# Kernel tuning notes

Hardware: AMD Instinct MI355X
Metric: run time of the kernel (lower is better)

## Reference

```python
import jax, jax.numpy as jnp
import numpy as np

D_MODEL = 512
N_HEADS = 8
HEAD_DIM = D_MODEL // N_HEADS
SEQ = 2048
BATCH = 2
EPS = 1e-5
SCALE = 1.0 / np.sqrt(HEAD_DIM).astype(np.float32)
# (kind, window, dilation) per head, matching init_kwargs head_specs
SPECS = [("global", 0, 1), ("global", 0, 1),
         ("window", 64, 1), ("window", 128, 1), ("window", 256, 1),
         ("dilated", 64, 2), ("dilated", 64, 4), ("dilated", 64, 8)]


def build_masks(N):
    i = jnp.arange(N)
    D = jnp.abs(i[:, None] - i[None, :])
    ms = []
    for kind, w, dil in SPECS:
        if kind == "global":
            ms.append(jnp.ones((N, N), dtype=bool))
        elif kind == "window":
            ms.append(D <= w)
        else:  # dilated
            ms.append((D % dil == 0) & (D // dil <= w))
    return jnp.stack(ms)  # [H, N, N] bool


def layernorm(x, g, b):
    mu = jnp.mean(x, axis=-1, keepdims=True)
    var = jnp.mean((x - mu) ** 2, axis=-1, keepdims=True)
    return (x - mu) * jax.lax.rsqrt(var + EPS) * g + b


def setup_inputs() -> dict:
    key = jax.random.key(0)
    ks = jax.random.split(key, 7)
    w = 0.02
    return {
        "x": jax.random.normal(ks[0], (BATCH, SEQ, D_MODEL), dtype=jnp.float32),
        "Wq": jax.random.normal(ks[1], (D_MODEL, D_MODEL), dtype=jnp.float32) * w,
        "Wk": jax.random.normal(ks[2], (D_MODEL, D_MODEL), dtype=jnp.float32) * w,
        "Wv": jax.random.normal(ks[3], (D_MODEL, D_MODEL), dtype=jnp.float32) * w,
        "Wo": jax.random.normal(ks[4], (D_MODEL, D_MODEL), dtype=jnp.float32) * w,
        "T_w1": jax.random.normal(ks[5], (D_MODEL, D_MODEL), dtype=jnp.float32) * w,
        "T_b1": jnp.zeros((D_MODEL,), dtype=jnp.float32),
        "T_w2": jax.random.normal(ks[6], (1, D_MODEL), dtype=jnp.float32) * w,
        "T_b2": jnp.zeros((1,), dtype=jnp.float32),
        "ln_in_g": jnp.ones((D_MODEL,), dtype=jnp.float32),
        "ln_in_b": jnp.zeros((D_MODEL,), dtype=jnp.float32),
        "ln_out_g": jnp.ones((D_MODEL,), dtype=jnp.float32),
        "ln_out_b": jnp.zeros((D_MODEL,), dtype=jnp.float32),
    }


def reference(x, Wq, Wk, Wv, Wo, T_w1, T_b1, T_w2, T_b2,
              ln_in_g, ln_in_b, ln_out_g, ln_out_b):
    B, N, H = x.shape
    x0 = x
    xn = layernorm(x, ln_in_g, ln_in_b)
    # torch Linear: y = x @ W.T ; reshape to [B, h, N, d]
    def heads(W):
        return (xn @ W.T).reshape(B, N, N_HEADS, HEAD_DIM).transpose(0, 2, 1, 3)
    Q, K, V = heads(Wq), heads(Wk), heads(Wv)
    attn = jnp.einsum("bhqd,bhkd->bhqk", Q, K) * SCALE
    mask = build_masks(N)  # [h, N, N]
    attn = jnp.where(mask[None], attn, -jnp.inf)
    attn = jax.nn.softmax(attn, axis=-1)  # every row has diagonal unmasked
    out = jnp.einsum("bhqk,bhkd->bhqd", attn, V)
    out = out.transpose(0, 2, 1, 3).reshape(B, N, N_HEADS * HEAD_DIM)
    out = out @ Wo.T
    # tanh-gated softmax over sequence dim
    T_logits = jnp.tanh(xn @ T_w1.T + T_b1) @ T_w2.T + T_b2  # [B, N, 1]
    T = jax.nn.softmax(T_logits, axis=1)
    out = out * T
    return layernorm(out + x0, ln_out_g, ln_out_b)
```

## Files before the change

### kernel.cpp

```cpp
#include <hip/hip_runtime.h>
#include <math.h>

#define N_SEQ 2048
#define DM    512
#define NTOK  4096
#define NH    8
#define HD    64
#define NSLOT 18

typedef __attribute__((ext_vector_type(8))) short short8;
typedef __attribute__((ext_vector_type(4))) short short4_t;
typedef __attribute__((ext_vector_type(4))) float f32x4;

__device__ inline short f2bf(float x) {
    union { float f; unsigned u; } v; v.f = x;
    unsigned r = v.u + 0x7fff + ((v.u >> 16) & 1);
    return (short)(r >> 16);
}
__device__ inline float bf2f(short s) {
    union { unsigned u; float f; } v; v.u = ((unsigned)(unsigned short)s) << 16;
    return v.f;
}
__device__ inline unsigned pkbf(float a, float b) {
    return ((unsigned)(unsigned short)f2bf(b) << 16) | (unsigned)(unsigned short)f2bf(a);
// ... 32 lines not shown
        __shared__ float ls[4], lq[4];
        if ((t & 63) == 0) { ls[t >> 6] = s; lq[t >> 6] = q; }
        __syncthreads();
        s = ls[sub * 2] + ls[sub * 2 + 1];
        q = lq[sub * 2] + lq[sub * 2 + 1];
        float mu = s * (1.f / DM);
        float var = q * (1.f / DM) - mu * mu;
        float rs = rsqrtf(var + 1e-5f);
        float4 gv = ((const float4*)g)[tt], bv = ((const float4*)b)[tt];
        short4_t o;
        o[0] = f2bf((xv.x - mu) * rs * gv.x + bv.x);
        o[1] = f2bf((xv.y - mu) * rs * gv.y + bv.y);
        o[2] = f2bf((xv.z - mu) * rs * gv.z + bv.z);
        o[3] = f2bf((xv.w - mu) * rs * gv.w + bv.w);
        *(short4_t*)&y[(size_t)tk * DM + tt * 4] = o;
    } else {
        int id = (blk - 2048) * 256 + t;
        if (id < 262144) {
            int z = id >> 16; int off = id & 65535;
            const float* s = (z == 0) ? Wq : (z == 1) ? Wk : (z == 2) ? Wv : Tw1;
            float4 v = ((const float4*)s)[off];
            short4_t o = {f2bf(v.x), f2bf(v.y), f2bf(v.z), f2bf(v.w)};
            *(short4_t*)(wcat + (size_t)z * 262144 + (size_t)off * 4) = o;
        } else {
            int off = id - 262144;
            float4 v = ((const float4*)Wo)[off];
            short4_t o = {f2bf(v.x), f2bf(v.y), f2bf(v.z), f2bf(v.w)};
            *(short4_t*)(wo + (size_t)off * 4) = o;
        }
    }
}

__global__ __launch_bounds__(256) void k_gemmqkvt(
    const short* __restrict__ A, const short* __restrict__ W,
    const float* __restrict__ Tb1, const float* __restrict__ Tw2,
    short* __restrict__ qb, short* __restrict__ kb, short* __restrict__ vtb,
    float* __restrict__ lg) {
    __shared__ short smem[17408];
    int t = threadIdx.x;
    int lane = t & 63, w = t >> 6;
    int wy = w >> 1, wx = w & 1;
    int ln = lane & 15, q4 = lane >> 4;
    int c0 = blockIdx.x * 128, m0 = blockIdx.y * 128;
    int sr = t >> 2, sc = (t & 3) << 3;
    f32x4 acc[4][4];
    f32x4 zero = {0.f, 0.f, 0.f, 0.f};
    #pragma unroll
    for (int i = 0; i < 4; i++)
        #pragma unroll
        for (int j = 0; j < 4; j++) acc[i][j] = zero;
    {
        short* AsB = smem; short* BsB = smem + 4096;
        async_cp16(&A[(size_t)(m0 + sr) * DM + sc],      &AsB[sr * 32 + sc]);
        async_cp16(&A[(size_t)(m0 + 64 + sr) * DM + sc], &AsB[(64 + sr) * 32 + sc]);
        async_cp16(&W[(size_t)(c0 + sr) * DM + sc],      &BsB[sr * 32 + sc]);
        async_cp16(&W[(size_t)(c0 + 64 + sr) * DM + sc], &BsB[(64 + sr) * 32 + sc]);
    }
    __syncthreads();
    for (int kk = 0; kk < 16; kk++) {
        short* AsB = &smem[(kk & 1) * 8192];
        short* BsB = AsB + 4096;
        if (kk < 15) {
            short* AsN = &smem[((kk & 1) ^ 1) * 8192];
            short* BsN = AsN + 4096;
            int k0 = (kk + 1) * 32;
            async_cp16(&A[(size_t)(m0 + sr) * DM + k0 + sc],      &AsN[sr * 32 + sc]);
            async_cp16(&A[(size_t)(m0 + 64 + sr) * DM + k0 + sc], &AsN[(64 + sr) * 32 + sc]);
            async_cp16(&W[(size_t)(c0 + sr) * DM + k0 + sc],      &BsN[sr * 32 + sc]);
            async_cp16(&W[(size_t)(c0 + 64 + sr) * DM + k0 + sc], &BsN[(64 + sr) * 32 + sc]);
        }
        short8 af[4], bfr[4];
        #pragma unroll
        for (int i = 0; i < 4; i++)
            af[i] = *(short8*)&AsB[(wy * 64 + i * 16 + ln) * 32 + q4 * 8];
        #pragma unroll
        for (int j = 0; j < 4; j++)
            bfr[j] = *(short8*)&BsB[(wx * 64 + j * 16 + ln) * 32 + q4 * 8];
        #pragma unroll
        for (int i = 0; i < 4; i++)
            #pragma unroll
            for (int j = 0; j < 4; j++)
                acc[i][j] = mfma16(af[i], bfr[j], acc[i][j]);
        __syncthreads();
    }
    short* Es = smem;
    int z = c0 >> 9;
    int bi = m0 >> 11, n0 = m0 & (N_SEQ - 1);
    int hp = (c0 & 511) >> 6;
    if (z < 2) {
        short* dst0 = (z == 0) ? qb : kb;
        float sc2 = (z == 0) ? 0.125f : 1.0f;
        #pragma unroll
        for (int i = 0; i < 4; i++)
            #pragma unroll
            for (int j = 0; j < 4; j++)
                #pragma unroll
                for (int r = 0; r < 4; r++) {
                    int nl = wy * 64 + i * 16 + q4 * 4 + r;
                    int cl = wx * 64 + j * 16 + ln;
                    Es[nl * 136 + cl] = f2bf(acc[i][j][r] * sc2);
                }
        __syncthreads();
        #pragma unroll
        for (int ii = 0; ii < 8; ii++) {
            int id = t + 256 * ii;
            int nl = id >> 4, c8 = id & 15;
            short8 v = *(short8*)&Es[nl * 136 + c8 * 8];
            int hh = hp + (c8 >> 3), d8 = (c8 & 7) * 8;
            *(short8*)&dst0[(((size_t)bi * NH + hh) * N_SEQ + n0 + nl) * HD + d8] = v;
        }
    } else if (z == 2) {
        #pragma unroll
        for (int i = 0; i < 4; i++)
            #pragma unroll
            for (int j = 0; j < 4; j++) {
                int nl0 = wy * 64 + i * 16 + q4 * 4;
                int dl = wx * 64 + j * 16 + ln;
                *(unsigned*)&Es[dl * 136 + nl0]     = pkbf(acc[i][j][0], acc[i][j][1]);
                *(unsigned*)&Es[dl * 136 + nl0 + 2] = pkbf(acc[i][j][2], acc[i][j][3]);
            }
        __syncthreads();
        #pragma unroll
        for (int ii = 0; ii < 8; ii++) {
            int id = t + 256 * ii;
            int dl = id >> 4, nc = id & 15;
            short8 v = *(short8*)&Es[dl * 136 + nc * 8];
            int h = hp + (dl >> 6), d = dl & 63;
            *(short8*)&vtb[(((size_t)bi * NH + h) * HD + d) * N_SEQ + n0 + nc * 8] = v;
        }
    } else {
        #pragma unroll
        for (int i = 0; i < 4; i++) {
            #pragma unroll
            for (int r = 0; r < 4; r++) {
                float s = 0.f;
                #pragma unroll
                for (int j = 0; j < 4; j++) {
                    int tc = (c0 & 511) + wx * 64 + j * 16 + ln;
                    s += ftanh(acc[i][j][r] + Tb1[tc]) * Tw2[tc];
                }
                s += __shfl_xor(s, 1);
                s += __shfl_xor(s, 2);
                s += __shfl_xor(s, 4);
                s += __shfl_xor(s, 8);
                if (ln == 0) {
                    int row = m0 + wy * 64 + i * 16 + q4 * 4 + r;
                    atomicAdd(&lg[row], s);
                }
            }
        }
    }
}

__global__ __launch_bounds__(256) void k_gemmp(
    const short* __restrict__ A, const short* __restrict__ W,
    float* __restrict__ proj) {
    __shared__ short smem[12288];
    int t = threadIdx.x;
    int lane = t & 63, w = t >> 6;
    int wy = w >> 1, wx = w & 1;
    int ln = lane & 15, q4 = lane >> 4;
    int c0 = blockIdx.x * 64, m0 = blockIdx.y * 128;
    int sr = t >> 2, sc = (t & 3) << 3;
    f32x4 acc[4][2];
    f32x4 zero = {0.f, 0.f, 0.f, 0.f};
    #pragma unroll
    for (int i = 0; i < 4; i++) { acc[i][0] = zero; acc[i][1] = zero; }
    {
        short* AsB = smem; short* BsB = smem + 4096;
        async_cp16(&A[(size_t)(m0 + sr) * DM + sc],      &AsB[sr * 32 + sc]);
        async_cp16(&A[(size_t)(m0 + 64 + sr) * DM + sc], &AsB[(64 + sr) * 32 + sc]);
        async_cp16(&W[(size_t)(c0 + sr) * DM + sc],      &BsB[sr * 32 + sc]);
    }
    __syncthreads();
    for (int kk = 0; kk < 16; kk++) {
        short* AsB = &smem[(kk & 1) * 6144];
        short* BsB = AsB + 4096;
        if (kk < 15) {
            short* AsN = &smem[((kk & 1) ^ 1) * 6144];
            short* BsN = AsN + 4096;
            int k0 = (kk + 1) * 32;
            async_cp16(&A[(size_t)(m0 + sr) * DM + k0 + sc],      &AsN[sr * 32 + sc]);
            async_cp16(&A[(size_t)(m0 + 64 + sr) * DM + k0 + sc], &AsN[(64 + sr) * 32 + sc]);
            async_cp16(&W[(size_t)(c0 + sr) * DM + k0 + sc],      &BsN[sr * 32 + sc]);
        }
        short8 af[4], bfr[2];
        #pragma unroll
        for (int i = 0; i < 4; i++)
            af[i] = *(short8*)&AsB[(wy * 64 + i * 16 + ln) * 32 + q4 * 8];
        #pragma unroll
        for (int j = 0; j < 2; j++)
            bfr[j] = *(short8*)&BsB[(wx * 32 + j * 16 + ln) * 32 + q4 * 8];
        #pragma unroll
        for (int i = 0; i < 4; i++)
            #pragma unroll
            for (int j = 0; j < 2; j++)
                acc[i][j] = mfma16(af[i], bfr[j], acc[i][j]);
        __syncthreads();
    }
    #pragma unroll
    for (int i = 0; i < 4; i++)
        #pragma unroll
        for (int j = 0; j < 2; j++)
            #pragma unroll
            for (int r = 0; r < 4; r++) {
                int row = m0 + wy * 64 + i * 16 + q4 * 4 + r;
                int col = c0 + wx * 32 + j * 16 + ln;
                proj[(size_t)row * DM + col] = acc[i][j][r];
            }
}

__global__ __launch_bounds__(256) void k_attn(const short* __restrict__ qb,
                                              const short* __restrict__ kb,
                                              const short* __restrict__ vtb,
                                              short* __restrict__ P_O,
                                              float* __restrict__ P_ml,
                                              short* __restrict__ ob,
                                              const float* __restrict__ lg,
                                              float* __restrict__ gate) {
    __shared__ short Ks[128 * 64];
    __shared__ short Vt[64 * 128];
    __shared__ short Pa[4][16 * 136];
    __shared__ float rg[8];
    int t = threadIdx.x;
    int lane = t & 63, w = t >> 6;
    int ln = lane & 15, q4 = lane >> 4;
    int slot = blockIdx.x, qt = blockIdx.y, bi = blockIdx.z;
    int q0 = qt * 64;
    int h, c;
    if (slot < 4)        { h = 0; c = slot; }
    else if (slot < 8)   { h = 1; c = slot - 4; }
    else if (slot == 8)  { h = 2; c = 0; }
    else if (slot == 9)  { h = 3; c = 0; }
    else if (slot < 12)  { h = 4; c = slot - 10; }
    else if (slot == 12) { h = 5; c = 0; }
    else if (slot < 15)  { h = 6; c = slot - 13; }
    else                 { h = 7; c = slot - 15; }
    int solo = (slot == 8) | (slot == 9) | (slot == 12);
    int kind = (h < 2) ? 0 : (h < 5) ? 1 : 2;
    int wnd = (h == 2 || h >= 5) ? 64 : (h == 3) ? 128 : (h == 4) ? 256 : 0;
    int dsh = (h == 5) ? 1 : (h == 6) ? 2 : (h == 7) ? 3 : 0;
    int dmask = (1 << dsh) - 1;
    int wmax = (kind == 0) ? 0 : (wnd << dsh);
    int tLoU, tHiU, CS;
    if (kind == 0) { tLoU = 0; tHiU = 15; CS = 4; }
    else { tLoU = (q0 - wmax) >> 7; tHiU = (q0 + 63 + wmax) >> 7; CS = 3; }
    int ktLo = tLoU + c * CS;
    int ktHi = ktLo + CS - 1;
    if (ktHi > tHiU) ktHi = tHiU;
    if (ktHi > 15) ktHi = 15;
    if (ktLo < 0) ktLo = 0;
    int p4 = (bi * 32 + qt) * NSLOT + slot;
    float* ml = P_ml + (size_t)p4 * 128;
    if (ktLo > ktHi) {
        if (t < 64) { ml[t] = -1e30f; ml[64 + t] = 0.f; }
        return;
    }
    const size_t base = ((size_t)bi * NH + h) * N_SEQ * HD;
    const short* Q = qb + base;
    const short* K = kb + base;
    const short* Vg = vtb + base;
    short8 qa[2];
    {
        const short* qrow = Q + (size_t)(q0 + w * 16 + ln) * HD + q4 * 8;
        qa[0] = *(const short8*)qrow;
        qa[1] = *(const short8*)(qrow + 32);
    }
    int qi = q0 + w * 16 + ln;
    float m_i = -1e30f, l_i = 0.f;
    f32x4 OT[4];
    f32x4 zero = {0.f, 0.f, 0.f, 0.f};
    #pragma unroll
    for (int d = 0; d < 4; d++) OT[d] = zero;
    short* Paw = Pa[w];
    for (int kt = ktLo; kt <= ktHi; kt++) {
        int k0 = kt << 7;
        __syncthreads();
        #pragma unroll
        for (int i2 = 0; i2 < 4; i2++) {
            int id = t + 256 * i2;
            int kr = id >> 3, ck = id & 7;
            async_cp16(&K[(size_t)(k0 + kr) * HD + ((ck ^ (kr & 7)) << 3)],
                       &Ks[id << 3]);
            int dr = id >> 4, cv = id & 15;
            async_cp16(&Vg[(size_t)dr * N_SEQ + k0 + ((cv ^ (dr & 15)) << 3)],
                       &Vt[id << 3]);
        }
        __syncthreads();
        f32x4 ST[8];
        #pragma unroll
        for (int nt = 0; nt < 8; nt++) ST[nt] = zero;
        __builtin_amdgcn_s_setprio(1);
        #pragma unroll
        for (int nt = 0; nt < 8; nt++) {
            #pragma unroll
            for (int ks = 0; ks < 2; ks++) {
                int cc = ((ks * 4 + q4) ^ (ln & 7)) << 3;
                short8 af = *(short8*)&Ks[(nt * 16 + ln) * 64 + cc];
                ST[nt] = mfma16(af, qa[ks], ST[nt]);
            }
        }
        __builtin_amdgcn_s_setprio(0);
        if (kind != 0) {
            #pragma unroll
            for (int nt = 0; nt < 8; nt++)
                #pragma unroll
                for (int r = 0; r < 4; r++) {
                    int key = k0 + nt * 16 + q4 * 4 + r;
                    int dlt = qi - key; dlt = (dlt < 0) ? -dlt : dlt;
                    int valid;
                    if (kind == 1) valid = (dlt <= wnd);
                    else valid = ((dlt & dmask) == 0) && ((dlt >> dsh) <= wnd);
                    if (!valid) ST[nt][r] = -1e30f;
                }
        }
        float rm = -1e30f;
        #pragma unroll
        for (int nt = 0; nt < 8; nt++) {
            float a = fmaxf(ST[nt][0], ST[nt][1]);
            float b = fmaxf(ST[nt][2], ST[nt][3]);
            rm = fmaxf(rm, fmaxf(a, b));
        }
        rm = fmaxf(rm, __shfl_xor(rm, 16));
        rm = fmaxf(rm, __shfl_xor(rm, 32));
        float mn = fmaxf(m_i, rm);
        float sc = __expf(m_i - mn);
        float rs = 0.f;
        #pragma unroll
        for (int nt = 0; nt < 8; nt++) {
            float p0 = __expf(ST[nt][0] - mn);
            float p1 = __expf(ST[nt][1] - mn);
            float p2 = __expf(ST[nt][2] - mn);
            float p3 = __expf(ST[nt][3] - mn);
            rs += (p0 + p1) + (p2 + p3);
            *(unsigned*)&Paw[ln * 136 + nt * 16 + q4 * 4]     = pkbf(p0, p1);
            *(unsigned*)&Paw[ln * 136 + nt * 16 + q4 * 4 + 2] = pkbf(p2, p3);
        }
        rs += __shfl_xor(rs, 16);
        rs += __shfl_xor(rs, 32);
        l_i = l_i * sc + rs;
        m_i = mn;
        #pragma unroll
        for (int d = 0; d < 4; d++) OT[d] *= sc;
        short8 pb[4];
        #pragma unroll
        for (int ks = 0; ks < 4; ks++)
            pb[ks] = *(short8*)&Paw[ln * 136 + ks * 32 + q4 * 8];
        __builtin_amdgcn_s_setprio(1);
        #pragma unroll
        for (int dt = 0; dt < 4; dt++) {
            #pragma unroll
            for (int ks = 0; ks < 4; ks++) {
                int cc = ((ks * 4 + q4) ^ ln) << 3;
                short8 a = *(short8*)&Vt[(dt * 16 + ln) * 128 + cc];
                OT[dt] = mfma16(a, pb[ks], OT[dt]);
            }
        }
        __builtin_amdgcn_s_setprio(0);
    }
    if (solo) {
        float inv = 1.f / l_i;
        #pragma unroll
        for (int dt = 0; dt < 4; dt++) {
            *(unsigned*)&Paw[ln * 136 + dt * 16 + q4 * 4]     = pkbf(OT[dt][0] * inv, OT[dt][1] * inv);
            *(unsigned*)&Paw[ln * 136 + dt * 16 + q4 * 4 + 2] = pkbf(OT[dt][2] * inv, OT[dt][3] * inv);
        }
        short8 o0 = *(short8*)&Paw[ln * 136 + q4 * 16];
        short8 o1 = *(short8*)&Paw[ln * 136 + q4 * 16 + 8];
        short* dst = ob + ((size_t)bi * N_SEQ + q0 + w * 16 + ln) * DM + h * 64 + q4 * 16;
        *(short8*)dst = o0;
        *(short8*)(dst + 8) = o1;
    } else {
        if (q4 == 0) { ml[w * 16 + ln] = m_i; ml[64 + w * 16 + ln] = l_i; }
        #pragma unroll
        for (int dt = 0; dt < 4; dt++) {
            *(unsigned*)&Paw[ln * 136 + dt * 16 + q4 * 4]     = pkbf(OT[dt][0], OT[dt][1]);
            *(unsigned*)&Paw[ln * 136 + dt * 16 + q4 * 4 + 2] = pkbf(OT[dt][2], OT[dt][3]);
        }
        short8 o0 = *(short8*)&Paw[ln * 136 + q4 * 16];
        short8 o1 = *(short8*)&Paw[ln * 136 + q4 * 16 + 8];
        short* Op = P_O + (size_t)p4 * 4096;
        *(short8*)&Op[(w * 16 + ln) * 64 + q4 * 16] = o0;
        *(short8*)&Op[(w * 16 + ln) * 64 + q4 * 16 + 8] = o1;
    }
    if (slot == 8 && qt == 0) {
        int b = bi;
        float v[8];
        float4 a0 = *(const float4*)&lg[b * N_SEQ + t * 8];
        float4 a1 = *(const float4*)&lg[b * N_SEQ + t * 8 + 4];
        v[0] = a0.x; v[1] = a0.y; v[2] = a0.z; v[3] = a0.w;
        v[4] = a1.x; v[5] = a1.y; v[6] = a1.z; v[7] = a1.w;
        float m = v[0];
        #pragma unroll
        for (int j = 1; j < 8; j++) m = fmaxf(m, v[j]);
        for (int o = 32; o; o >>= 1) m = fmaxf(m, __shfl_down(m, o));
        if ((t & 63) == 0) rg[t >> 6] = m;
        __syncthreads();
        m = fmaxf(fmaxf(rg[0], rg[1]), fmaxf(rg[2], rg[3]));
        float e[8], s = 0.f;
        #pragma unroll
        for (int j = 0; j < 8; j++) { e[j] = __expf(v[j] - m); s += e[j]; }
        for (int o = 32; o; o >>= 1) s += __shfl_down(s, o);
        if ((t & 63) == 0) rg[4 + (t >> 6)] = s;
        __syncthreads();
        s = (rg[4] + rg[5]) + (rg[6] + rg[7]);
        float inv = 1.f / s;
        float4 o0 = {e[0] * inv, e[1] * inv, e[2] * inv, e[3] * inv};
        float4 o1 = {e[4] * inv, e[5] * inv, e[6] * inv, e[7] * inv};
        *(float4*)&gate[b * N_SEQ + t * 8] = o0;
        *(float4*)&gate[b * N_SEQ + t * 8 + 4] = o1;
    }
}

__global__ __launch_bounds__(256) void k_combine(const short* __restrict__ P_O,
                                                 const float* __restrict__ P_ml,
                                                 short* __restrict__ ob) {
    const int hsel[5]  = {0, 1, 4, 6, 7};
    const int hbase[5] = {0, 4, 10, 13, 15};
    const int hcnt[5]  = {4, 4, 2, 2, 3};
    int hh = blockIdx.x, qt = blockIdx.y, bi = blockIdx.z;
    int h = hsel[hh];
    int t = threadIdx.x;
    int row = t >> 2, c0 = (t & 3) * 16;
    int pb = (bi * 32 + qt) * NSLOT + hbase[hh];
    int cnt = hcnt[hh];
    float m = -1e30f;
    for (int s = 0; s < cnt; s++)
        m = fmaxf(m, P_ml[(size_t)(pb + s) * 128 + row]);
    float l = 0.f;
    float acc[16];
    #pragma unroll
    for (int j = 0; j < 16; j++) acc[j] = 0.f;
    for (int s = 0; s < cnt; s++) {
        float ms = P_ml[(size_t)(pb + s) * 128 + row];
        float ls = P_ml[(size_t)(pb + s) * 128 + 64 + row];
        if (ls > 0.f) {
            float sc = __expf(ms - m);
            l += ls * sc;
            const short* Op = P_O + (size_t)(pb + s) * 4096 + row * 64 + c0;
            short8 v0 = *(const short8*)Op;
            short8 v1 = *(const short8*)(Op + 8);
            #pragma unroll
            for (int j = 0; j < 8; j++) acc[j]     += bf2f(v0[j]) * sc;
            #pragma unroll
            for (int j = 0; j < 8; j++) acc[8 + j] += bf2f(v1[j]) * sc;
        }
    }
    float inv = 1.f / l;
    int n = qt * 64 + row;
    short8 o0, o1;
    #pragma unroll
    for (int j = 0; j < 8; j++) o0[j] = f2bf(acc[j] * inv);
    #pragma unroll
    for (int j = 0; j < 8; j++) o1[j] = f2bf(acc[8 + j] * inv);
    short* dst = ob + ((size_t)bi * N_SEQ + n) * DM + h * 64 + c0;
    *(short8*)dst = o0;
    *(short8*)(dst + 8) = o1;
}

__global__ __launch_bounds__(128) void k_final(const float* __restrict__ proj,
                                               const float* __restrict__ gate,
                                               const float* __restrict__ x0,
                                               const float* __restrict__ g,
                                               const float* __restrict__ b,
                                               float* __restrict__ out) {
    int tk = blockIdx.x, t = threadIdx.x;
    float gt = gate[tk];
    float4 pv = ((const float4*)(proj + (size_t)tk * DM))[t];
    float4 xv = ((const float4*)(x0 + (size_t)tk * DM))[t];
    float4 y;
    y.x = pv.x * gt + xv.x;
    y.y = pv.y * gt + xv.y;
    y.z = pv.z * gt + xv.z;
    y.w = pv.w * gt + xv.w;
    float s = y.x + y.y + y.z + y.w;
    float q = y.x*y.x + y.y*y.y + y.z*y.z + y.w*y.w;
    for (int o = 32; o; o >>= 1) { s += __shfl_down(s, o); q += __shfl_down(q, o); }
    __shared__ float ls[2], lq[2];
    if ((t & 63) == 0) { ls[t >> 6] = s; lq[t >> 6] = q; }
    __syncthreads();
    s = ls[0] + ls[1]; q = lq[0] + lq[1];
    float mu = s * (1.f / DM);
    float var = q * (1.f / DM) - mu * mu;
    float rs = rsqrtf(var + 1e-5f);
    float4 gv = ((const float4*)g)[t], bv = ((const float4*)b)[t];
    float4 o;
    o.x = (y.x - mu) * rs * gv.x + bv.x;
    o.y = (y.y - mu) * rs * gv.y + bv.y;
    o.z = (y.z - mu) * rs * gv.z + bv.z;
    o.w = (y.w - mu) * rs * gv.w + bv.w;
    ((float4*)(out + (size_t)tk * DM))[t] = o;
}

extern "C" void kernel_launch(void* const* d_in, const int* in_sizes, int n_in,
                              void* d_out, int out_size, void* d_ws, size_t ws_size,
                              hipStream_t stream) {
    (void)in_sizes; (void)n_in; (void)out_size; (void)ws_size;
    const float* x    = (const float*)d_in[0];
    const float* Wq   = (const float*)d_in[1];
    const float* Wk   = (const float*)d_in[2];
    const float* Wv   = (const float*)d_in[3];
    const float* Wo   = (const float*)d_in[4];
    const float* Tw1  = (const float*)d_in[5];
    const float* Tb1  = (const float*)d_in[6];
    const float* Tw2  = (const float*)d_in[7];
    const float* ling = (const float*)d_in[9];
    const float* linb = (const float*)d_in[10];
    const float* logg = (const float*)d_in[11];
    const float* logb = (const float*)d_in[12];
    float* out = (float*)d_out;

    const size_t SZ = (size_t)NTOK * DM;
    const int NPART = 2 * 32 * NSLOT;
    char* p = (char*)d_ws;
    short* xn   = (short*)p; p += SZ * 2;
    short* wcat = (short*)p; p += (size_t)2048 * DM * 2;
    short* wo   = (short*)p; p += (size_t)DM * DM * 2;
    short* qb   = (short*)p; p += SZ * 2;
    short* kb   = (short*)p; p += SZ * 2;
    short* vtb  = (short*)p; p += SZ * 2;
    short* obuf = (short*)p; p += SZ * 2;
    float* lg   = (float*)p; p += (size_t)NTOK * 4;
    float* gate = (float*)p; p += (size_t)NTOK * 4;
    float* P_ml = (float*)p; p += (size_t)NPART * 128 * 4;
    float* proj = (float*)p;
    short* P_O  = (short*)p; p += (size_t)NPART * 4096 * 2;

    k_lncvt<<<3328, 256, 0, stream>>>(x, ling, linb, xn, lg,
                                      Wq, Wk, Wv, Tw1, Wo, wcat, wo);
    k_gemmqkvt<<<dim3(16, 32), 256, 0, stream>>>(xn, wcat, Tb1, Tw2,
                                                 qb, kb, vtb, lg);
    k_attn<<<dim3(NSLOT, 32, 2), 256, 0, stream>>>(qb, kb, vtb, P_O, P_ml,
                                                   obuf, lg, gate);
    k_combine<<<dim3(5, 32, 2), 256, 0, stream>>>(P_O, P_ml, obuf);
    k_gemmp<<<dim3(8, 32), 256, 0, stream>>>(obuf, wo, proj);
    k_final<<<NTOK, 128, 0, stream>>>(proj, gate, x, logg, logb, out);
}
```

Before: 154.5 us.

## Fuse split-KV combine, output projection, gating and final layernorm into one kernel

Drops the separate combine, output-projection GEMM and final layernorm kernels and replaces them with a single kernel. Each 512-thread block merges the partial attention results for 64 rows across all heads into shared memory, multiplies them by Wo, applies the gate and residual, and performs the layernorm in registers. Solo-head attention slots no longer write normalized output directly; they now write partials like the other slots. This removes two launches and the obuf/proj round trips through global memory. The cost is that the fused kernel runs only 64 blocks with a large shared-memory footprint, so GPU occupancy and parallelism drop sharply.

```diff
diff --git a/kernel.cpp b/kernel.cpp
--- a/kernel.cpp
+++ b/kernel.cpp
@@ -208,70 +208,11 @@
     }
 }
 
-__global__ __launch_bounds__(256) void k_gemmp(
-    const short* __restrict__ A, const short* __restrict__ W,
-    float* __restrict__ proj) {
-    __shared__ short smem[12288];
-    int t = threadIdx.x;
-    int lane = t & 63, w = t >> 6;
-    int wy = w >> 1, wx = w & 1;
-    int ln = lane & 15, q4 = lane >> 4;
-    int c0 = blockIdx.x * 64, m0 = blockIdx.y * 128;
-    int sr = t >> 2, sc = (t & 3) << 3;
-    f32x4 acc[4][2];
-    f32x4 zero = {0.f, 0.f, 0.f, 0.f};
-    #pragma unroll
-    for (int i = 0; i < 4; i++) { acc[i][0] = zero; acc[i][1] = zero; }
-    {
-        short* AsB = smem; short* BsB = smem + 4096;
-        async_cp16(&A[(size_t)(m0 + sr) * DM + sc],      &AsB[sr * 32 + sc]);
-        async_cp16(&A[(size_t)(m0 + 64 + sr) * DM + sc], &AsB[(64 + sr) * 32 + sc]);
-        async_cp16(&W[(size_t)(c0 + sr) * DM + sc],      &BsB[sr * 32 + sc]);
-    }
-    __syncthreads();
-    for (int kk = 0; kk < 16; kk++) {
-        short* AsB = &smem[(kk & 1) * 6144];
-        short* BsB = AsB + 4096;
-        if (kk < 15) {
-            short* AsN = &smem[((kk & 1) ^ 1) * 6144];
-            short* BsN = AsN + 4096;
-            int k0 = (kk + 1) * 32;
-            async_cp16(&A[(size_t)(m0 + sr) * DM + k0 + sc],      &AsN[sr * 32 + sc]);
-            async_cp16(&A[(size_t)(m0 + 64 + sr) * DM + k0 + sc], &AsN[(64 + sr) * 32 + sc]);
-            async_cp16(&W[(size_t)(c0 + sr) * DM + k0 + sc],      &BsN[sr * 32 + sc]);
-        }
-        short8 af[4], bfr[2];
-        #pragma unroll
-        for (int i = 0; i < 4; i++)
-            af[i] = *(short8*)&AsB[(wy * 64 + i * 16 + ln) * 32 + q4 * 8];
-        #pragma unroll
-        for (int j = 0; j < 2; j++)
-            bfr[j] = *(short8*)&BsB[(wx * 32 + j * 16 + ln) * 32 + q4 * 8];
-        #pragma unroll
-        for (int i = 0; i < 4; i++)
-            #pragma unroll
-            for (int j = 0; j < 2; j++)
-                acc[i][j] = mfma16(af[i], bfr[j], acc[i][j]);
-        __syncthreads();
-    }
-    #pragma unroll
-    for (int i = 0; i < 4; i++)
-        #pragma unroll
-        for (int j = 0; j < 2; j++)
-            #pragma unroll
-            for (int r = 0; r < 4; r++) {
-                int row = m0 + wy * 64 + i * 16 + q4 * 4 + r;
-                int col = c0 + wx * 32 + j * 16 + ln;
-                proj[(size_t)row * DM + col] = acc[i][j][r];
-            }
-}
-
 __global__ __launch_bounds__(256) void k_attn(const short* __restrict__ qb,
                                               const short* __restrict__ kb,
                                               const short* __restrict__ vtb,
                                               short* __restrict__ P_O,
                                               float* __restrict__ P_ml,
-                                              short* __restrict__ ob,
                                               const float* __restrict__ lg,
                                               float* __restrict__ gate) {
     __shared__ short Ks[128 * 64];
@@ -292,7 +233,6 @@
     else if (slot == 12) { h = 5; c = 0; }
     else if (slot < 15)  { h = 6; c = slot - 13; }
     else                 { h = 7; c = slot - 15; }
-    int solo = (slot == 8) | (slot == 9) | (slot == 12);
     int kind = (h < 2) ? 0 : (h < 5) ? 1 : 2;
     int wnd = (h == 2 || h >= 5) ? 64 : (h == 3) ? 128 : (h == 4) ? 256 : 0;
     int dsh = (h == 5) ? 1 : (h == 6) ? 2 : (h == 7) ? 3 : 0;
@@ -308,125 +248,114 @@
     if (ktLo < 0) ktLo = 0;
     int p4 = (bi * 32 + qt) * NSLOT + slot;
     float* ml = P_ml + (size_t)p4 * 128;
-    if (ktLo > ktHi) {
+    int empty = (ktLo > ktHi);
+    if (empty) {
         if (t < 64) { ml[t] = -1e30f; ml[64 + t] = 0.f; }
-        return;
+        if (!(slot == 8 && qt == 0)) return;
     }
     const size_t base = ((size_t)bi * NH + h) * N_SEQ * HD;
     const short* Q = qb + base;
     const short* K = kb + base;
     const short* Vg = vtb + base;
-    short8 qa[2];
-    {
-        const short* qrow = Q + (size_t)(q0 + w * 16 + ln) * HD + q4 * 8;
-        qa[0] = *(const short8*)qrow;
-        qa[1] = *(const short8*)(qrow + 32);
-    }
-    int qi = q0 + w * 16 + ln;
-    float m_i = -1e30f, l_i = 0.f;
-    f32x4 OT[4];
-    f32x4 zero = {0.f, 0.f, 0.f, 0.f};
-    #pragma unroll
-    for (int d = 0; d < 4; d++) OT[d] = zero;
-    short* Paw = Pa[w];
-    for (int kt = ktLo; kt <= ktHi; kt++) {
-        int k0 = kt << 7;
-        __syncthreads();
-        #pragma unroll
-        for (int i2 = 0; i2 < 4; i2++) {
-            int id = t + 256 * i2;
-            int kr = id >> 3, ck = id & 7;
-            async_cp16(&K[(size_t)(k0 + kr) * HD + ((ck ^ (kr & 7)) << 3)],
-                       &Ks[id << 3]);
-            int dr = id >> 4, cv = id & 15;
-            async_cp16(&Vg[(size_t)dr * N_SEQ + k0 + ((cv ^ (dr & 15)) << 3)],
-                       &Vt[id << 3]);
-        }
-        __syncthreads();
-        f32x4 ST[8];
-        #pragma unroll
-        for (int nt = 0; nt < 8; nt++) ST[nt] = zero;
-        __builtin_amdgcn_s_setprio(1);
-        #pragma unroll
-        for (int nt = 0; nt < 8; nt++) {
-            #pragma unroll
-            for (int ks = 0; ks < 2; ks++) {
-                int cc = ((ks * 4 + q4) ^ (ln & 7)) << 3;
-                short8 af = *(short8*)&Ks[(nt * 16 + ln) * 64 + cc];
-                ST[nt] = mfma16(af, qa[ks], ST[nt]);
-            }
-        }
-        __builtin_amdgcn_s_setprio(0);
-        if (kind != 0) {
-            #pragma unroll
-            for (int nt = 0; nt < 8; nt++)
+    if (!empty) {
+        short8 qa[2];
+        {
+            const short* qrow = Q + (size_t)(q0 + w * 16 + ln) * HD + q4 * 8;
+            qa[0] = *(const short8*)qrow;
+            qa[1] = *(const short8*)(qrow + 32);
+        }
+        int qi = q0 + w * 16 + ln;
+        float m_i = -1e30f, l_i = 0.f;
+        f32x4 OT[4];
+        f32x4 zero = {0.f, 0.f, 0.f, 0.f};
+        #pragma unroll
+        for (int d = 0; d < 4; d++) OT[d] = zero;
+        short* Paw = Pa[w];
+        for (int kt = ktLo; kt <= ktHi; kt++) {
+            int k0 = kt << 7;
+            __syncthreads();
+            #pragma unroll
+            for (int i2 = 0; i2 < 4; i2++) {
+                int id = t + 256 * i2;
+                int kr = id >> 3, ck = id & 7;
+                async_cp16(&K[(size_t)(k0 + kr) * HD + ((ck ^ (kr & 7)) << 3)],
+                           &Ks[id << 3]);
+                int dr = id >> 4, cv = id & 15;
+                async_cp16(&Vg[(size_t)dr * N_SEQ + k0 + ((cv ^ (dr & 15)) << 3)],
+                           &Vt[id << 3]);
+            }
+            __syncthreads();
+            f32x4 ST[8];
+            #pragma unroll
+            for (int nt = 0; nt < 8; nt++) ST[nt] = zero;
+            __builtin_amdgcn_s_setprio(1);
+            #pragma unroll
+            for (int nt = 0; nt < 8; nt++) {
                 #pragma unroll
-                for (int r = 0; r < 4; r++) {
-                    int key = k0 + nt * 16 + q4 * 4 + r;
-                    int dlt = qi - key; dlt = (dlt < 0) ? -dlt : dlt;
-                    int valid;
-                    if (kind == 1) valid = (dlt <= wnd);
-                    else valid = ((dlt & dmask) == 0) && ((dlt >> dsh) <= wnd);
-                    if (!valid) ST[nt][r] = -1e30f;
+                for (int ks = 0; ks < 2; ks++) {
+                    int cc = ((ks * 4 + q4) ^ (ln & 7)) << 3;
+                    short8 af = *(short8*)&Ks[(nt * 16 + ln) * 64 + cc];
+                    ST[nt] = mfma16(af, qa[ks], ST[nt]);
                 }
-        }
-        float rm = -1e30f;
-        #pragma unroll
-        for (int nt = 0; nt < 8; nt++) {
-            float a = fmaxf(ST[nt][0], ST[nt][1]);
-            float b = fmaxf(ST[nt][2], ST[nt][3]);
-            rm = fmaxf(rm, fmaxf(a, b));
-        }
-        rm = fmaxf(rm, __shfl_xor(rm, 16));
-        rm = fmaxf(rm, __shfl_xor(rm, 32));
-        float mn = fmaxf(m_i, rm);
-        float sc = __expf(m_i - mn);
-        float rs = 0.f;
-        #pragma unroll
-        for (int nt = 0; nt < 8; nt++) {
-            float p0 = __expf(ST[nt][0] - mn);
-            float p1 = __expf(ST[nt][1] - mn);
-            float p2 = __expf(ST[nt][2] - mn);
-            float p3 = __expf(ST[nt][3] - mn);
-            rs += (p0 + p1) + (p2 + p3);
-            *(unsigned*)&Paw[ln * 136 + nt * 16 + q4 * 4]     = pkbf(p0, p1);
-            *(unsigned*)&Paw[ln * 136 + nt * 16 + q4 * 4 + 2] = pkbf(p2, p3);
-        }
-        rs += __shfl_xor(rs, 16);
-        rs += __shfl_xor(rs, 32);
-        l_i = l_i * sc + rs;
-        m_i = mn;
-        #pragma unroll
-        for (int d = 0; d < 4; d++) OT[d] *= sc;
-        short8 pb[4];
-        #pragma unroll
-        for (int ks = 0; ks < 4; ks++)
-            pb[ks] = *(short8*)&Paw[ln * 136 + ks * 32 + q4 * 8];
-        __builtin_amdgcn_s_setprio(1);
-        #pragma unroll
-        for (int dt = 0; dt < 4; dt++) {
-            #pragma unroll
-            for (int ks = 0; ks < 4; ks++) {
-                int cc = ((ks * 4 + q4) ^ ln) << 3;
-                short8 a = *(short8*)&Vt[(dt * 16 + ln) * 128 + cc];
-                OT[dt] = mfma16(a, pb[ks], OT[dt]);
-            }
-        }
-        __builtin_amdgcn_s_setprio(0);
-    }
-    if (solo) {
-        float inv = 1.f / l_i;
-        #pragma unroll
-        for (int dt = 0; dt < 4; dt++) {
-            *(unsigned*)&Paw[ln * 136 + dt * 16 + q4 * 4]     = pkbf(OT[dt][0] * inv, OT[dt][1] * inv);
-            *(unsigned*)&Paw[ln * 136 + dt * 16 + q4 * 4 + 2] = pkbf(OT[dt][2] * inv, OT[dt][3] * inv);
-        }
-        short8 o0 = *(short8*)&Paw[ln * 136 + q4 * 16];
-        short8 o1 = *(short8*)&Paw[ln * 136 + q4 * 16 + 8];
-        short* dst = ob + ((size_t)bi * N_SEQ + q0 + w * 16 + ln) * DM + h * 64 + q4 * 16;
-        *(short8*)dst = o0;
-        *(short8*)(dst + 8) = o1;
-    } else {
+            }
+            __builtin_amdgcn_s_setprio(0);
+            if (kind != 0) {
+                #pragma unroll
+                for (int nt = 0; nt < 8; nt++)
+                    #pragma unroll
+                    for (int r = 0; r < 4; r++) {
+                        int key = k0 + nt * 16 + q4 * 4 + r;
+                        int dlt = qi - key; dlt = (dlt < 0) ? -dlt : dlt;
+                        int valid;
+                        if (kind == 1) valid = (dlt <= wnd);
+                        else valid = ((dlt & dmask) == 0) && ((dlt >> dsh) <= wnd);
+                        if (!valid) ST[nt][r] = -1e30f;
+                    }
+            }
+            float rm = -1e30f;
+            #pragma unroll
+            for (int nt = 0; nt < 8; nt++) {
+                float a = fmaxf(ST[nt][0], ST[nt][1]);
+                float b = fmaxf(ST[nt][2], ST[nt][3]);
+                rm = fmaxf(rm, fmaxf(a, b));
+            }
+            rm = fmaxf(rm, __shfl_xor(rm, 16));
+            rm = fmaxf(rm, __shfl_xor(rm, 32));
+            float mn = fmaxf(m_i, rm);
+            float sc = __expf(m_i - mn);
+            float rs = 0.f;
+            #pragma unroll
+            for (int nt = 0; nt < 8; nt++) {
+                float p0 = __expf(ST[nt][0] - mn);
+                float p1 = __expf(ST[nt][1] - mn);
+                float p2 = __expf(ST[nt][2] - mn);
+                float p3 = __expf(ST[nt][3] - mn);
+                rs += (p0 + p1) + (p2 + p3);
+                *(unsigned*)&Paw[ln * 136 + nt * 16 + q4 * 4]     = pkbf(p0, p1);
+                *(unsigned*)&Paw[ln * 136 + nt * 16 + q4 * 4 + 2] = pkbf(p2, p3);
+            }
+            rs += __shfl_xor(rs, 16);
+            rs += __shfl_xor(rs, 32);
+            l_i = l_i * sc + rs;
+            m_i = mn;
+            #pragma unroll
+            for (int d = 0; d < 4; d++) OT[d] *= sc;
+            short8 pb[4];
+            #pragma unroll
+            for (int ks = 0; ks < 4; ks++)
+                pb[ks] = *(short8*)&Paw[ln * 136 + ks * 32 + q4 * 8];
+            __builtin_amdgcn_s_setprio(1);
+            #pragma unroll
+            for (int dt = 0; dt < 4; dt++) {
+                #pragma unroll
+                for (int ks = 0; ks < 4; ks++) {
+                    int cc = ((ks * 4 + q4) ^ ln) << 3;
+                    short8 a = *(short8*)&Vt[(dt * 16 + ln) * 128 + cc];
+                    OT[dt] = mfma16(a, pb[ks], OT[dt]);
+                }
+            }
+            __builtin_amdgcn_s_setprio(0);
+        }
         if (q4 == 0) { ml[w * 16 + ln] = m_i; ml[64 + w * 16 + ln] = l_i; }
         #pragma unroll
         for (int dt = 0; dt < 4; dt++) {
@@ -468,84 +397,156 @@
     }
 }
 
-__global__ __launch_bounds__(256) void k_combine(const short* __restrict__ P_O,
-                                                 const float* __restrict__ P_ml,
-                                                 short* __restrict__ ob) {
-    const int hsel[5]  = {0, 1, 4, 6, 7};
-    const int hbase[5] = {0, 4, 10, 13, 15};
-    const int hcnt[5]  = {4, 4, 2, 2, 3};
-    int hh = blockIdx.x, qt = blockIdx.y, bi = blockIdx.z;
-    int h = hsel[hh];
+__global__ __launch_bounds__(512) void k_cgf(
+    const short* __restrict__ P_O, const float* __restrict__ P_ml,
+    const short* __restrict__ wo, const float* __restrict__ gate,
+    const float* __restrict__ x0, const float* __restrict__ g,
+    const float* __restrict__ b, float* __restrict__ out) {
+    __shared__ short As[64 * 512];
+    __shared__ short Bs[2][512 * 32];
+    __shared__ float red[8][64][2];
+    __shared__ float rowp[64][2];
+    __shared__ float gsm[64];
     int t = threadIdx.x;
-    int row = t >> 2, c0 = (t & 3) * 16;
-    int pb = (bi * 32 + qt) * NSLOT + hbase[hh];
-    int cnt = hcnt[hh];
-    float m = -1e30f;
-    for (int s = 0; s < cnt; s++)
-        m = fmaxf(m, P_ml[(size_t)(pb + s) * 128 + row]);
-    float l = 0.f;
-    float acc[16];
-    #pragma unroll
-    for (int j = 0; j < 16; j++) acc[j] = 0.f;
-    for (int s = 0; s < cnt; s++) {
-        float ms = P_ml[(size_t)(pb + s) * 128 + row];
-        float ls = P_ml[(size_t)(pb + s) * 128 + 64 + row];
-        if (ls > 0.f) {
-            float sc = __expf(ms - m);
-            l += ls * sc;
-            const short* Op = P_O + (size_t)(pb + s) * 4096 + row * 64 + c0;
-            short8 v0 = *(const short8*)Op;
-            short8 v1 = *(const short8*)(Op + 8);
-            #pragma unroll
-            for (int j = 0; j < 8; j++) acc[j]     += bf2f(v0[j]) * sc;
-            #pragma unroll
-            for (int j = 0; j < 8; j++) acc[8 + j] += bf2f(v1[j]) * sc;
-        }
-    }
-    float inv = 1.f / l;
-    int n = qt * 64 + row;
-    short8 o0, o1;
-    #pragma unroll
-    for (int j = 0; j < 8; j++) o0[j] = f2bf(acc[j] * inv);
-    #pragma unroll
-    for (int j = 0; j < 8; j++) o1[j] = f2bf(acc[8 + j] * inv);
-    short* dst = ob + ((size_t)bi * N_SEQ + n) * DM + h * 64 + c0;
-    *(short8*)dst = o0;
-    *(short8*)(dst + 8) = o1;
-}
-
-__global__ __launch_bounds__(128) void k_final(const float* __restrict__ proj,
-                                               const float* __restrict__ gate,
-                                               const float* __restrict__ x0,
-                                               const float* __restrict__ g,
-                                               const float* __restrict__ b,
-                                               float* __restrict__ out) {
-    int tk = blockIdx.x, t = threadIdx.x;
-    float gt = gate[tk];
-    float4 pv = ((const float4*)(proj + (size_t)tk * DM))[t];
-    float4 xv = ((const float4*)(x0 + (size_t)tk * DM))[t];
-    float4 y;
-    y.x = pv.x * gt + xv.x;
-    y.y = pv.y * gt + xv.y;
-    y.z = pv.z * gt + xv.z;
-    y.w = pv.w * gt + xv.w;
-    float s = y.x + y.y + y.z + y.w;
-    float q = y.x*y.x + y.y*y.y + y.z*y.z + y.w*y.w;
-    for (int o = 32; o; o >>= 1) { s += __shfl_down(s, o); q += __shfl_down(q, o); }
-    __shared__ float ls[2], lq[2];
-    if ((t & 63) == 0) { ls[t >> 6] = s; lq[t >> 6] = q; }
+    int lane = t & 63, w = t >> 6;
+    int ln = lane & 15, q4 = lane >> 4;
+    int qt = blockIdx.x, bi = blockIdx.y;
+    int n0 = qt * 64;
+    const int hbase[8] = {0, 4, 8, 9, 10, 12, 13, 15};
+    const int hcnt[8]  = {4, 4, 1, 1, 2, 1, 2, 3};
+    int row = t >> 3, c8 = t & 7;
+    int pbb = (bi * 32 + qt) * NSLOT;
+    if (t < 64) gsm[t] = gate[bi * N_SEQ + n0 + t];
+    #pragma unroll
+    for (int h = 0; h < 8; h++) {
+        int pb = pbb + hbase[h], cnt = hcnt[h];
+        float m = -1e30f;
+        for (int s = 0; s < cnt; s++)
+            m = fmaxf(m, P_ml[(size_t)(pb + s) * 128 + row]);
+        float l = 0.f;
+        float a8[8];
+        #pragma unroll
+        for (int j = 0; j < 8; j++) a8[j] = 0.f;
+        for (int s = 0; s < cnt; s++) {
+            float ms = P_ml[(size_t)(pb + s) * 128 + row];
+            float ls = P_ml[(size_t)(pb + s) * 128 + 64 + row];
+            if (ls > 0.f) {
+                float sc = __expf(ms - m);
+                l += ls * sc;
+                short8 v = *(const short8*)&P_O[(size_t)(pb + s) * 4096 + row * 64 + c8 * 8];
+                #pragma unroll
+                for (int j = 0; j < 8; j++) a8[j] += bf2f(v[j]) * sc;
+            }
+        }
+        float inv = 1.f / l;
+        short8 o;
+        #pragma unroll
+        for (int j = 0; j < 8; j++) o[j] = f2bf(a8[j] * inv);
+        int chunk = (h << 3) | (c8 ^ (row & 7));
+        *(short8*)&As[row * 512 + chunk * 8] = o;
+    }
+    #pragma unroll
+    for (int i2 = 0; i2 < 4; i2++) {
+        int id = t + 512 * i2;
+        async_cp16(&wo[(size_t)(id >> 2) * 512 + ((id & 3) << 3)], &Bs[0][id * 8]);
+    }
     __syncthreads();
-    s = ls[0] + ls[1]; q = lq[0] + lq[1];
-    float mu = s * (1.f / DM);
-    float var = q * (1.f / DM) - mu * mu;
-    float rs = rsqrtf(var + 1e-5f);
-    float4 gv = ((const float4*)g)[t], bv = ((const float4*)b)[t];
-    float4 o;
-    o.x = (y.x - mu) * rs * gv.x + bv.x;
-    o.y = (y.y - mu) * rs * gv.y + bv.y;
-    o.z = (y.z - mu) * rs * gv.z + bv.z;
-    o.w = (y.w - mu) * rs * gv.w + bv.w;
-    ((float4*)(out + (size_t)tk * DM))[t] = o;
+    f32x4 acc[4][4];
+    f32x4 zero = {0.f, 0.f, 0.f, 0.f};
+    #pragma unroll
+    for (int i = 0; i < 4; i++)
+        #pragma unroll
+        for (int j = 0; j < 4; j++) acc[i][j] = zero;
+    for (int kk = 0; kk < 16; kk++) {
+        short* BsB = Bs[kk & 1];
+        if (kk < 15) {
+            int k0 = (kk + 1) * 32;
+            short* BsN = Bs[(kk & 1) ^ 1];
+            #pragma unroll
+            for (int i2 = 0; i2 < 4; i2++) {
+                int id = t + 512 * i2;
+                async_cp16(&wo[(size_t)(id >> 2) * 512 + k0 + ((id & 3) << 3)], &BsN[id * 8]);
+            }
+        }
+        short8 af[4], bfr[4];
+        #pragma unroll
+        for (int i = 0; i < 4; i++) {
+            int r2 = i * 16 + ln;
+            int chunk = (kk * 4 + q4) ^ (r2 & 7);
+            af[i] = *(short8*)&As[r2 * 512 + chunk * 8];
+        }
+        #pragma unroll
+        for (int j = 0; j < 4; j++)
+            bfr[j] = *(short8*)&BsB[(w * 64 + j * 16 + ln) * 32 + q4 * 8];
+        #pragma unroll
+        for (int i = 0; i < 4; i++)
+            #pragma unroll
+            for (int j = 0; j < 4; j++)
+                acc[i][j] = mfma16(af[i], bfr[j], acc[i][j]);
+        __syncthreads();
+    }
+    float sP[4][4], qP[4][4];
+    #pragma unroll
+    for (int i = 0; i < 4; i++)
+        #pragma unroll
+        for (int r = 0; r < 4; r++) { sP[i][r] = 0.f; qP[i][r] = 0.f; }
+    #pragma unroll
+    for (int i = 0; i < 4; i++)
+        #pragma unroll
+        for (int j = 0; j < 4; j++)
+            #pragma unroll
+            for (int r = 0; r < 4; r++) {
+                int rr = i * 16 + q4 * 4 + r;
+                int col = w * 64 + j * 16 + ln;
+                float y = acc[i][j][r] * gsm[rr] +
+                          x0[((size_t)(bi * N_SEQ + n0 + rr)) * DM + col];
+                acc[i][j][r] = y;
+                sP[i][r] += y; qP[i][r] += y * y;
+            }
+    #pragma unroll
+    for (int o = 1; o < 16; o <<= 1)
+        #pragma unroll
+        for (int i = 0; i < 4; i++)
+            #pragma unroll
+            for (int r = 0; r < 4; r++) {
+                sP[i][r] += __shfl_xor(sP[i][r], o);
+                qP[i][r] += __shfl_xor(qP[i][r], o);
+            }
+    if (ln == 0) {
+        #pragma unroll
+        for (int i = 0; i < 4; i++)
+            #pragma unroll
+            for (int r = 0; r < 4; r++) {
+                int rr = i * 16 + q4 * 4 + r;
+                red[w][rr][0] = sP[i][r];
+                red[w][rr][1] = qP[i][r];
+            }
+    }
+    __syncthreads();
+    if (t < 64) {
+        float s = 0.f, q = 0.f;
+        #pragma unroll
+        for (int w2 = 0; w2 < 8; w2++) { s += red[w2][t][0]; q += red[w2][t][1]; }
+        float mu = s * (1.f / DM);
+        float var = q * (1.f / DM) - mu * mu;
+        rowp[t][0] = mu;
+        rowp[t][1] = rsqrtf(var + 1e-5f);
+    }
+    __syncthreads();
+    #pragma unroll
+    for (int j = 0; j < 4; j++) {
+        int col = w * 64 + j * 16 + ln;
+        float gv = g[col], bv = b[col];
+        #pragma unroll
+        for (int i = 0; i < 4; i++)
+            #pragma unroll
+            for (int r = 0; r < 4; r++) {
+                int rr = i * 16 + q4 * 4 + r;
+                float mu = rowp[rr][0], rs = rowp[rr][1];
+                out[((size_t)(bi * N_SEQ + n0 + rr)) * DM + col] =
+                    (acc[i][j][r] - mu) * rs * gv + bv;
+            }
+    }
 }
 
 extern "C" void kernel_launch(void* const* d_in, const int* in_sizes, int n_in,
@@ -575,11 +576,9 @@
     short* qb   = (short*)p; p += SZ * 2;
     short* kb   = (short*)p; p += SZ * 2;
     short* vtb  = (short*)p; p += SZ * 2;
-    short* obuf = (short*)p; p += SZ * 2;
     float* lg   = (float*)p; p += (size_t)NTOK * 4;
     float* gate = (float*)p; p += (size_t)NTOK * 4;
     float* P_ml = (float*)p; p += (size_t)NPART * 128 * 4;
-    float* proj = (float*)p;
     short* P_O  = (short*)p; p += (size_t)NPART * 4096 * 2;
 
     k_lncvt<<<3328, 256, 0, stream>>>(x, ling, linb, xn, lg,
@@ -587,8 +586,7 @@
     k_gemmqkvt<<<dim3(16, 32), 256, 0, stream>>>(xn, wcat, Tb1, Tw2,
                                                  qb, kb, vtb, lg);
     k_attn<<<dim3(NSLOT, 32, 2), 256, 0, stream>>>(qb, kb, vtb, P_O, P_ml,
-                                                   obuf, lg, gate);
-    k_combine<<<dim3(5, 32, 2), 256, 0, stream>>>(P_O, P_ml, obuf);
-    k_gemmp<<<dim3(8, 32), 256, 0, stream>>>(obuf, wo, proj);
-    k_final<<<NTOK, 128, 0, stream>>>(proj, gate, x, logg, logb, out);
-}
+                                                   lg, gate);
+    k_cgf<<<dim3(32, 2), 512, 0, stream>>>(P_O, P_ml, wo, gate,
+                                           x, logg, logb, out);
+}
```

New measurement: 160.7 us. 4.0% more time.

## Enlarge attention query tile to 128 rows with 8-wave blocks

Applied to the files above, without the earlier changes.

The attention kernel now processes 128 query rows per block with 512 threads (8 waves) instead of 64 rows with 256 threads. Each K/V tile loaded into shared memory is reused by twice as many query rows, which halves the number of tiles loaded. The combine kernel, the partial buffers and the gate softmax are resized to match. The cost is half as many blocks, so fewer blocks run in parallel, and windowed heads may touch more key tiles per block.

```diff
diff --git a/kernel.cpp b/kernel.cpp
--- a/kernel.cpp
+++ b/kernel.cpp
@@ -266,7 +266,7 @@
             }
 }
 
-__global__ __launch_bounds__(256) void k_attn(const short* __restrict__ qb,
+__global__ __launch_bounds__(512) void k_attn(const short* __restrict__ qb,
                                               const short* __restrict__ kb,
                                               const short* __restrict__ vtb,
                                               short* __restrict__ P_O,
@@ -276,13 +276,13 @@
                                               float* __restrict__ gate) {
     __shared__ short Ks[128 * 64];
     __shared__ short Vt[64 * 128];
-    __shared__ short Pa[4][16 * 136];
-    __shared__ float rg[8];
+    __shared__ short Pa[8][16 * 136];
+    __shared__ float rg[16];
     int t = threadIdx.x;
     int lane = t & 63, w = t >> 6;
     int ln = lane & 15, q4 = lane >> 4;
     int slot = blockIdx.x, qt = blockIdx.y, bi = blockIdx.z;
-    int q0 = qt * 64;
+    int q0 = qt * 128;
     int h, c;
     if (slot < 4)        { h = 0; c = slot; }
     else if (slot < 8)   { h = 1; c = slot - 4; }
@@ -300,16 +300,16 @@
     int wmax = (kind == 0) ? 0 : (wnd << dsh);
     int tLoU, tHiU, CS;
     if (kind == 0) { tLoU = 0; tHiU = 15; CS = 4; }
-    else { tLoU = (q0 - wmax) >> 7; tHiU = (q0 + 63 + wmax) >> 7; CS = 3; }
+    else { tLoU = (q0 - wmax) >> 7; tHiU = (q0 + 127 + wmax) >> 7; CS = 3; }
     int ktLo = tLoU + c * CS;
     int ktHi = ktLo + CS - 1;
     if (ktHi > tHiU) ktHi = tHiU;
     if (ktHi > 15) ktHi = 15;
     if (ktLo < 0) ktLo = 0;
-    int p4 = (bi * 32 + qt) * NSLOT + slot;
-    float* ml = P_ml + (size_t)p4 * 128;
+    int p4 = (bi * 16 + qt) * NSLOT + slot;
+    float* ml = P_ml + (size_t)p4 * 256;
     if (ktLo > ktHi) {
-        if (t < 64) { ml[t] = -1e30f; ml[64 + t] = 0.f; }
+        if (t < 128) { ml[t] = -1e30f; ml[128 + t] = 0.f; }
         return;
     }
     const size_t base = ((size_t)bi * NH + h) * N_SEQ * HD;
@@ -333,13 +333,13 @@
         int k0 = kt << 7;
         __syncthreads();
         #pragma unroll
-        for (int i2 = 0; i2 < 4; i2++) {
-            int id = t + 256 * i2;
+        for (int i2 = 0; i2 < 2; i2++) {
+            int id = t + 512 * i2;
             int kr = id >> 3, ck = id & 7;
             async_cp16(&K[(size_t)(k0 + kr) * HD + ((ck ^ (kr & 7)) << 3)],
                        &Ks[id << 3]);
-            int dr = id >> 4, cv = id & 15;
-            async_cp16(&Vg[(size_t)dr * N_SEQ + k0 + ((cv ^ (dr & 15)) << 3)],
+            int dr = id >> 4, kc = id & 15;
+            async_cp16(&Vg[(size_t)dr * N_SEQ + k0 + ((kc ^ (dr & 15)) << 3)],
                        &Vt[id << 3]);
         }
         __syncthreads();
@@ -427,7 +427,7 @@
         *(short8*)dst = o0;
         *(short8*)(dst + 8) = o1;
     } else {
-        if (q4 == 0) { ml[w * 16 + ln] = m_i; ml[64 + w * 16 + ln] = l_i; }
+        if (q4 == 0) { ml[w * 16 + ln] = m_i; ml[128 + w * 16 + ln] = l_i; }
         #pragma unroll
         for (int dt = 0; dt < 4; dt++) {
             *(unsigned*)&Paw[ln * 136 + dt * 16 + q4 * 4]     = pkbf(OT[dt][0], OT[dt][1]);
@@ -435,36 +435,31 @@
         }
         short8 o0 = *(short8*)&Paw[ln * 136 + q4 * 16];
         short8 o1 = *(short8*)&Paw[ln * 136 + q4 * 16 + 8];
-        short* Op = P_O + (size_t)p4 * 4096;
+        short* Op = P_O + (size_t)p4 * 8192;
         *(short8*)&Op[(w * 16 + ln) * 64 + q4 * 16] = o0;
         *(short8*)&Op[(w * 16 + ln) * 64 + q4 * 16 + 8] = o1;
     }
     if (slot == 8 && qt == 0) {
         int b = bi;
-        float v[8];
-        float4 a0 = *(const float4*)&lg[b * N_SEQ + t * 8];
-        float4 a1 = *(const float4*)&lg[b * N_SEQ + t * 8 + 4];
-        v[0] = a0.x; v[1] = a0.y; v[2] = a0.z; v[3] = a0.w;
-        v[4] = a1.x; v[5] = a1.y; v[6] = a1.z; v[7] = a1.w;
-        float m = v[0];
-        #pragma unroll
-        for (int j = 1; j < 8; j++) m = fmaxf(m, v[j]);
+        float4 a0 = *(const float4*)&lg[b * N_SEQ + t * 4];
+        float v0 = a0.x, v1 = a0.y, v2 = a0.z, v3 = a0.w;
+        float m = fmaxf(fmaxf(v0, v1), fmaxf(v2, v3));
         for (int o = 32; o; o >>= 1) m = fmaxf(m, __shfl_down(m, o));
-        if ((t & 63) == 0) rg[t >> 6] = m;
-        __syncthreads();
-        m = fmaxf(fmaxf(rg[0], rg[1]), fmaxf(rg[2], rg[3]));
-        float e[8], s = 0.f;
-        #pragma unroll
-        for (int j = 0; j < 8; j++) { e[j] = __expf(v[j] - m); s += e[j]; }
+        if (lane == 0) rg[w] = m;
+        __syncthreads();
+        m = fmaxf(fmaxf(fmaxf(rg[0], rg[1]), fmaxf(rg[2], rg[3])),
+                  fmaxf(fmaxf(rg[4], rg[5]), fmaxf(rg[6], rg[7])));
+        float e0 = __expf(v0 - m), e1 = __expf(v1 - m);
+        float e2 = __expf(v2 - m), e3 = __expf(v3 - m);
+        float s = (e0 + e1) + (e2 + e3);
         for (int o = 32; o; o >>= 1) s += __shfl_down(s, o);
-        if ((t & 63) == 0) rg[4 + (t >> 6)] = s;
-        __syncthreads();
-        s = (rg[4] + rg[5]) + (rg[6] + rg[7]);
+        if (lane == 0) rg[8 + w] = s;
+        __syncthreads();
+        s = ((rg[8] + rg[9]) + (rg[10] + rg[11])) +
+            ((rg[12] + rg[13]) + (rg[14] + rg[15]));
         float inv = 1.f / s;
-        float4 o0 = {e[0] * inv, e[1] * inv, e[2] * inv, e[3] * inv};
-        float4 o1 = {e[4] * inv, e[5] * inv, e[6] * inv, e[7] * inv};
-        *(float4*)&gate[b * N_SEQ + t * 8] = o0;
-        *(float4*)&gate[b * N_SEQ + t * 8 + 4] = o1;
+        float4 o0 = {e0 * inv, e1 * inv, e2 * inv, e3 * inv};
+        *(float4*)&gate[b * N_SEQ + t * 4] = o0;
     }
 }
 
@@ -477,41 +472,45 @@
     int hh = blockIdx.x, qt = blockIdx.y, bi = blockIdx.z;
     int h = hsel[hh];
     int t = threadIdx.x;
-    int row = t >> 2, c0 = (t & 3) * 16;
-    int pb = (bi * 32 + qt) * NSLOT + hbase[hh];
+    int row0 = t >> 2, c0 = (t & 3) * 16;
+    int pb = (bi * 16 + qt) * NSLOT + hbase[hh];
     int cnt = hcnt[hh];
-    float m = -1e30f;
-    for (int s = 0; s < cnt; s++)
-        m = fmaxf(m, P_ml[(size_t)(pb + s) * 128 + row]);
-    float l = 0.f;
-    float acc[16];
     #pragma unroll
-    for (int j = 0; j < 16; j++) acc[j] = 0.f;
-    for (int s = 0; s < cnt; s++) {
-        float ms = P_ml[(size_t)(pb + s) * 128 + row];
-        float ls = P_ml[(size_t)(pb + s) * 128 + 64 + row];
-        if (ls > 0.f) {
-            float sc = __expf(ms - m);
-            l += ls * sc;
-            const short* Op = P_O + (size_t)(pb + s) * 4096 + row * 64 + c0;
-            short8 v0 = *(const short8*)Op;
-            short8 v1 = *(const short8*)(Op + 8);
-            #pragma unroll
-            for (int j = 0; j < 8; j++) acc[j]     += bf2f(v0[j]) * sc;
-            #pragma unroll
-            for (int j = 0; j < 8; j++) acc[8 + j] += bf2f(v1[j]) * sc;
-        }
-    }
-    float inv = 1.f / l;
-    int n = qt * 64 + row;
-    short8 o0, o1;
-    #pragma unroll
-    for (int j = 0; j < 8; j++) o0[j] = f2bf(acc[j] * inv);
-    #pragma unroll
-    for (int j = 0; j < 8; j++) o1[j] = f2bf(acc[8 + j] * inv);
-    short* dst = ob + ((size_t)bi * N_SEQ + n) * DM + h * 64 + c0;
-    *(short8*)dst = o0;
-    *(short8*)(dst + 8) = o1;
+    for (int half = 0; half < 2; half++) {
+        int row = half * 64 + row0;
+        float m = -1e30f;
+        for (int s = 0; s < cnt; s++)
+            m = fmaxf(m, P_ml[(size_t)(pb + s) * 256 + row]);
+        float l = 0.f;
+        float acc[16];
+        #pragma unroll
+        for (int j = 0; j < 16; j++) acc[j] = 0.f;
+        for (int s = 0; s < cnt; s++) {
+            float ms = P_ml[(size_t)(pb + s) * 256 + row];
+            float ls = P_ml[(size_t)(pb + s) * 256 + 128 + row];
+            if (ls > 0.f) {
+                float sc = __expf(ms - m);
+                l += ls * sc;
+                const short* Op = P_O + (size_t)(pb + s) * 8192 + row * 64 + c0;
+                short8 v0 = *(const short8*)Op;
+                short8 v1 = *(const short8*)(Op + 8);
+                #pragma unroll
+                for (int j = 0; j < 8; j++) acc[j]     += bf2f(v0[j]) * sc;
+                #pragma unroll
+                for (int j = 0; j < 8; j++) acc[8 + j] += bf2f(v1[j]) * sc;
+            }
+        }
+        float inv = 1.f / l;
+        int n = qt * 128 + row;
+        short8 o0, o1;
+        #pragma unroll
+        for (int j = 0; j < 8; j++) o0[j] = f2bf(acc[j] * inv);
+        #pragma unroll
+        for (int j = 0; j < 8; j++) o1[j] = f2bf(acc[8 + j] * inv);
+        short* dst = ob + ((size_t)bi * N_SEQ + n) * DM + h * 64 + c0;
+        *(short8*)dst = o0;
+        *(short8*)(dst + 8) = o1;
+    }
 }
 
 __global__ __launch_bounds__(128) void k_final(const float* __restrict__ proj,
@@ -567,7 +566,7 @@
     float* out = (float*)d_out;
 
     const size_t SZ = (size_t)NTOK * DM;
-    const int NPART = 2 * 32 * NSLOT;
+    const int NPART = 2 * 16 * NSLOT;
     char* p = (char*)d_ws;
     short* xn   = (short*)p; p += SZ * 2;
     short* wcat = (short*)p; p += (size_t)2048 * DM * 2;
@@ -578,17 +577,17 @@
     short* obuf = (short*)p; p += SZ * 2;
     float* lg   = (float*)p; p += (size_t)NTOK * 4;
     float* gate = (float*)p; p += (size_t)NTOK * 4;
-    float* P_ml = (float*)p; p += (size_t)NPART * 128 * 4;
+    float* P_ml = (float*)p; p += (size_t)NPART * 256 * 4;
     float* proj = (float*)p;
-    short* P_O  = (short*)p; p += (size_t)NPART * 4096 * 2;
+    short* P_O  = (short*)p; p += (size_t)NPART * 8192 * 2;
 
     k_lncvt<<<3328, 256, 0, stream>>>(x, ling, linb, xn, lg,
                                       Wq, Wk, Wv, Tw1, Wo, wcat, wo);
     k_gemmqkvt<<<dim3(16, 32), 256, 0, stream>>>(xn, wcat, Tb1, Tw2,
                                                  qb, kb, vtb, lg);
-    k_attn<<<dim3(NSLOT, 32, 2), 256, 0, stream>>>(qb, kb, vtb, P_O, P_ml,
+    k_attn<<<dim3(NSLOT, 16, 2), 512, 0, stream>>>(qb, kb, vtb, P_O, P_ml,
                                                    obuf, lg, gate);
-    k_combine<<<dim3(5, 32, 2), 256, 0, stream>>>(P_O, P_ml, obuf);
+    k_combine<<<dim3(5, 16, 2), 256, 0, stream>>>(P_O, P_ml, obuf);
     k_gemmp<<<dim3(8, 32), 256, 0, stream>>>(obuf, wo, proj);
     k_final<<<NTOK, 128, 0, stream>>>(proj, gate, x, logg, logb, out);
 }
```

Result: no change. 157.1 us (+1.7%).
